# Kernel optimization log

Measured on AMD Instinct MI355X. Metric: run time of the kernel, lower is better.

## Reference

```python
import math
import jax, jax.numpy as jnp
import numpy as np

N_QUBITS = 16
BATCH = 128
N_STATE = 2 ** N_QUBITS


def cnot_ring(n_qubits):
    """Permutation equivalent to a CNOT ring (faithful copy of the torch repo's numpy code)."""
    n2 = np.array([0, 2, 3, 1])
    if n_qubits == 2:
        return n2
    evens = np.zeros(2 ** (n_qubits - 1))
    answer = n2[::2]
    for i in range(1, n_qubits - 1):
        evens[:2 ** i] = answer
        a, b = np.array_split(answer, 2)
        evens[2 ** i:2 ** i + 2 ** (i - 1)] = a + 3 * 2 ** i
        evens[2 ** i + 2 ** (i - 1):2 ** (i + 1)] = b + 2 ** i
        answer = evens[:2 ** (i + 1)]
    a, b = np.split(evens.copy() + 2 ** (n_qubits - 2), 2)
    a = np.mod(a, 2 ** (n_qubits - 1))
    b, c = np.split(b, 2)
    b = b - 2 ** (n_qubits - 1)
    odds = np.concatenate((a, b, c), axis=0)[::-1]
    output = np.zeros(2 ** n_qubits)
    output[::2] = evens
    output[1::2] = odds
    return output.astype(int)


def binary_mask(n_qubits):
    """[n, 2**n] matrix; row i is bit (n-1-i from LSB) of the column index,
    matching torch binary_matrix (dim 0 of the [2]*n tensor is the MSB)."""
    idx = jnp.arange(2 ** n_qubits, dtype=jnp.int32)
    shifts = (n_qubits - 1 - jnp.arange(n_qubits, dtype=jnp.int32))
    return ((idx[None, :] >> shifts[:, None]) & 1).astype(jnp.float32)


def wht(x):
    """Walsh-Hadamard transform over the last dim of [B, N] complex state (had_big butterfly)."""
    B, N = x.shape
    n = int(math.log2(N))
    for i in range(n):
        x = x.reshape(B, 2 ** i, 2, N >> (i + 1))
        a, b = x[:, :, 0, :], x[:, :, 1, :]
        x = jnp.stack([a + b, a - b], axis=2)
    return x.reshape(B, N) * jnp.asarray(2.0 ** (-n / 2), dtype=x.dtype)


def setup_inputs() -> dict:
    key = jax.random.key(0)
    k1, k2, k3 = jax.random.split(key, 3)
    state_re = jax.random.normal(k1, (BATCH, N_STATE), dtype=jnp.float32)
    state_im = jax.random.normal(k2, (BATCH, N_STATE), dtype=jnp.float32)
    thetas = jax.random.normal(k3, (BATCH, N_QUBITS), dtype=jnp.float32)
    cnot_p = jnp.asarray(cnot_ring(N_QUBITS), dtype=jnp.int32)
    return {"state_re": state_re, "state_im": state_im, "thetas": thetas, "cnot_p": cnot_p}


def reference(state_re, state_im, thetas, cnot_p):
    # set_state('random'): l2-normalize complex state per batch row
    norm = jnp.sqrt(jnp.sum(state_re * state_re + state_im * state_im, axis=-1, keepdims=True))
    state = (state_re + 1j * state_im) / norm  # complex64 [B, N]
    # hadamard layer (had_big WHT butterfly)
    state = wht(state)
    # RZ layer: thetas @ binary mask -> phase eigenvalues exp(-i*theta/2)
    ang = thetas @ binary_mask(N_QUBITS)  # [B, N]
    state = state * jnp.exp(-0.5j * ang)
    # CNOT ring: gather permutation over the state axis
    state = state[:, cnot_p]
    # second hadamard layer
    state = wht(state)
    # measure(): probabilities |psi|^2
    return jnp.abs(state) ** 2
```

## Files before the change

kernel.cpp:

```cpp
#include <hip/hip_runtime.h>
#include <hip/hip_fp16.h>

#define NB 128
#define NS 65536

typedef float v2f __attribute__((ext_vector_type(2)));

__device__ __forceinline__ v2f pk_fma(v2f a, v2f b, v2f c) {
  v2f d;
  asm("v_pk_fma_f32 %0, %1, %2, %3" : "=v"(d) : "v"(a), "v"(b), "v"(c));
  return d;
}
__device__ __forceinline__ v2f pk_add(v2f a, v2f b) {
  v2f d;
  asm("v_pk_add_f32 %0, %1, %2" : "=v"(d) : "v"(a), "v"(b));
  return d;
}
__device__ __forceinline__ v2f pk_mul(v2f a, v2f b) {
  v2f d;
  asm("v_pk_mul_f32 %0, %1, %2" : "=v"(d) : "v"(a), "v"(b));
  return d;
}

template <int CTRL>
__device__ __forceinline__ float dppmov(float x) {
  return __int_as_float(__builtin_amdgcn_update_dpp(
      0, __float_as_int(x), CTRL, 0xF, 0xF, false));
}
__device__ __forceinline__ float xor4mov(float x) {
  int t = __builtin_amdgcn_update_dpp(0, __float_as_int(x), 0x104, 0xF, 0x5, false);
  t = __builtin_amdgcn_update_dpp(t, __float_as_int(x), 0x114, 0xF, 0xA, false);
  return __int_as_float(t);
}

__device__ __forceinline__ void wht256p(v2f (&p)[4], int lane) {
  const v2f M1 = {-1.f, -1.f};
  {
    v2f t;
    t = p[0]; p[0] = pk_add(t, p[1]); p[1] = pk_fma(M1, p[1], t);
    t = p[2]; p[2] = pk_add(t, p[3]); p[3] = pk_fma(M1, p[3], t);
    t = p[0]; p[0] = pk_add(t, p[2]); p[2] = pk_fma(M1, p[2], t);
    t = p[1]; p[1] = pk_add(t, p[3]); p[3] = pk_fma(M1, p[3], t);
  }
  const float s1f  = (lane & 1)  ? -1.f : 1.f;
  const float s2f  = (lane & 2)  ? -1.f : 1.f;
  const float s4f  = (lane & 4)  ? -1.f : 1.f;
  const float s8f  = (lane & 8)  ? -1.f : 1.f;
  const float s16f = (lane & 16) ? -1.f : 1.f;
  const float s32f = (lane & 32) ? -1.f : 1.f;
  const v2f s1 = {s1f, s1f}, s2 = {s2f, s2f}, s4 = {s4f, s4f};
  const v2f s8 = {s8f, s8f}, s16 = {s16f, s16f}, s32 = {s32f, s32f};
#pragma unroll
  for (int q = 0; q < 4; ++q) {
    v2f m = {dppmov<0xB1>(p[q].x), dppmov<0xB1>(p[q].y)};
    p[q] = pk_fma(s1, p[q], m);
  }
#pragma unroll
  for (int q = 0; q < 4; ++q) {
    v2f m = {dppmov<0x4E>(p[q].x), dppmov<0x4E>(p[q].y)};
    p[q] = pk_fma(s2, p[q], m);
  }
#pragma unroll
  for (int q = 0; q < 4; ++q) {
    v2f m = {xor4mov(p[q].x), xor4mov(p[q].y)};
    p[q] = pk_fma(s4, p[q], m);
  }
#pragma unroll
  for (int q = 0; q < 4; ++q) {
    v2f m = {dppmov<0x128>(p[q].x), dppmov<0x128>(p[q].y)};
    p[q] = pk_fma(s8, p[q], m);
  }
#pragma unroll
  for (int q = 0; q < 4; ++q) {
    auto rre = __builtin_amdgcn_permlane16_swap(__float_as_uint(p[q].x),
                                                __float_as_uint(p[q].x), false, false);
    auto rim = __builtin_amdgcn_permlane16_swap(__float_as_uint(p[q].y),
                                                __float_as_uint(p[q].y), false, false);
    v2f lo = {__uint_as_float(rre[0]), __uint_as_float(rim[0])};
    v2f hi = {__uint_as_float(rre[1]), __uint_as_float(rim[1])};
    p[q] = pk_fma(s16, hi, lo);
  }
#pragma unroll
  for (int q = 0; q < 4; ++q) {
    auto rre = __builtin_amdgcn_permlane32_swap(__float_as_uint(p[q].x),
                                                __float_as_uint(p[q].x), false, false);
    auto rim = __builtin_amdgcn_permlane32_swap(__float_as_uint(p[q].y),
                                                __float_as_uint(p[q].y), false, false);
    v2f lo = {__uint_as_float(rre[0]), __uint_as_float(rim[0])};
    v2f hi = {__uint_as_float(rre[1]), __uint_as_float(rim[1])};
    p[q] = pk_fma(s32, hi, lo);
  }
}

__global__ __launch_bounds__(1024, 8) void k1_ahi(const float* __restrict__ sre,
                                                  const float* __restrict__ sim,
                                                  const float* __restrict__ thetas,
                                                  __half* __restrict__ T,
                                                  float* __restrict__ partial) {
  __shared__ float sr[32][260];
  __shared__ float si[32][260];
  __shared__ float2 phh4[64];
  __shared__ float2 phHQ[4];
  __shared__ float red[16];
  const int bid = blockIdx.x;
  const int b = bid >> 3, tile = bid & 7;
  const int lo0 = tile * 32;
  const int tid = threadIdx.x, lane = tid & 63, w = tid >> 6;
  if (tid < 64) {
    const float* tb = thetas + b * 16;
    float a = 0.f;
#pragma unroll
    for (int i = 0; i < 6; ++i)
      if ((tid >> (5 - i)) & 1) a += tb[i];
    phh4[tid] = make_float2(cosf(0.5f * a), -sinf(0.5f * a));
    if (tid < 4) {
      float aq = 0.f;
      if (tid & 1) aq += tb[7];
      if (tid & 2) aq += tb[6];
      phHQ[tid] = make_float2(cosf(0.5f * aq), -sinf(0.5f * aq));
    }
  }
  const float* pre = sre + ((size_t)b << 16);
  const float* pim = sim + ((size_t)b << 16);
  const int c = tid & 7, jr = tid >> 3;
  const int j0 = jr, j1 = jr + 128;
  const float4 vr0 = *reinterpret_cast<const float4*>(pre + j0 * 256 + lo0 + c * 4);
  const float4 vi0 = *reinterpret_cast<const float4*>(pim + j0 * 256 + lo0 + c * 4);
  const float4 vr1 = *reinterpret_cast<const float4*>(pre + j1 * 256 + lo0 + c * 4);
  const float4 vi1 = *reinterpret_cast<const float4*>(pim + j1 * 256 + lo0 + c * 4);
  float acc = vr0.x*vr0.x + vr0.y*vr0.y + vr0.z*vr0.z + vr0.w*vr0.w
            + vi0.x*vi0.x + vi0.y*vi0.y + vi0.z*vi0.z + vi0.w*vi0.w
            + vr1.x*vr1.x + vr1.y*vr1.y + vr1.z*vr1.z + vr1.w*vr1.w
            + vi1.x*vi1.x + vi1.y*vi1.y + vi1.z*vi1.z + vi1.w*vi1.w;
  {
    const int fs = ((c >> 1) & 3) << 2;
    const int j0s = j0 ^ fs, j1s = j1 ^ fs;
    sr[c*4+0][j0s] = vr0.x; sr[c*4+1][j0s] = vr0.y; sr[c*4+2][j0s] = vr0.z; sr[c*4+3][j0s] = vr0.w;
    si[c*4+0][j0s] = vi0.x; si[c*4+1][j0s] = vi0.y; si[c*4+2][j0s] = vi0.z; si[c*4+3][j0s] = vi0.w;
    sr[c*4+0][j1s] = vr1.x; sr[c*4+1][j1s] = vr1.y; sr[c*4+2][j1s] = vr1.z; sr[c*4+3][j1s] = vr1.w;
    si[c*4+0][j1s] = vi1.x; si[c*4+1][j1s] = vi1.y; si[c*4+2][j1s] = vi1.z; si[c*4+3][j1s] = vi1.w;
  }
#pragma unroll
  for (int m2 = 32; m2 >= 1; m2 >>= 1) acc += __shfl_xor(acc, m2, 64);
  if (lane == 0) red[w] = acc;
  __syncthreads();
  if (tid == 0) {
    float sm = 0.f;
#pragma unroll
    for (int k = 0; k < 16; ++k) sm += red[k];
    partial[bid] = sm;
  }
  const float2 p4 = phh4[lane];
  float prq[4], piq[4];
#pragma unroll
  for (int q = 0; q < 4; ++q) {
    const float2 pq = phHQ[q];
    prq[q] = p4.x * pq.x - p4.y * pq.y;
    piq[q] = p4.x * pq.y + p4.y * pq.x;
  }
#pragma unroll
  for (int r = 0; r < 2; ++r) {
    const int ll = w * 2 + r;
    const int blk = lane ^ ((ll >> 3) & 3);
    const float4 a4 = *reinterpret_cast<const float4*>(&sr[ll][blk * 4]);
    const float4 b4 = *reinterpret_cast<const float4*>(&si[ll][blk * 4]);
    v2f p[4] = {{a4.x, b4.x}, {a4.y, b4.y}, {a4.z, b4.z}, {a4.w, b4.w}};
    wht256p(p, lane);
#pragma unroll
    for (int q = 0; q < 4; ++q) {
      const float ur = p[q].x, ui = p[q].y;
      const v2f tt = pk_mul(p[q], (v2f){prq[q], prq[q]});
      p[q].x = fmaf(-piq[q], ui, tt.x);
      p[q].y = fmaf(piq[q], ur, tt.y);
    }
    wht256p(p, lane);
    *reinterpret_cast<float4*>(&sr[ll][blk * 4]) =
        make_float4(p[0].x, p[1].x, p[2].x, p[3].x);
    *reinterpret_cast<float4*>(&si[ll][blk * 4]) =
        make_float4(p[0].y, p[1].y, p[2].y, p[3].y);
  }
  __syncthreads();
  __half* Tb = T + ((size_t)b << 17);
  const int m = tid >> 2, sub = tid & 3;
  const int ms = m ^ (sub << 2);
  unsigned int o8[8];
#pragma unroll
  for (int t = 0; t < 8; ++t) {
    const int ll = 8 * sub + t;
    const __half2 h = __floats2half2_rn(sr[ll][ms], si[ll][ms]);
    o8[t] = *reinterpret_cast<const unsigned int*>(&h);
  }
  __half* dst = Tb + ((size_t)m << 9) + (size_t)(lo0 + 8 * sub) * 2;
  *reinterpret_cast<uint4*>(dst) = make_uint4(o8[0], o8[1], o8[2], o8[3]);
  *reinterpret_cast<uint4*>(dst + 8) = make_uint4(o8[4], o8[5], o8[6], o8[7]);
}

__global__ __launch_bounds__(256, 8) void k2_alo_scatter(const __half* __restrict__ T,
                                                         const float* __restrict__ thetas,
                                                         const int* __restrict__ cnot,
                                                         const float* __restrict__ partial,
                                                         float* __restrict__ outp) {
  __shared__ float2 phl4[64];
  __shared__ float2 phLQ[4];
  __shared__ int sloL[64];
  __shared__ int tj[16];
  __shared__ int srow16[16];
  __shared__ float th[16];
  __shared__ float shinv;
  const int bid = blockIdx.x;
  const int x = bid & 7, s2i = bid >> 3;
  const int b = x * 16 + (s2i >> 4), tile = s2i & 15;
  const int tid = threadIdx.x, lane = tid & 63, w = tid >> 6;
  if (tid < 16) {
    th[tid] = thetas[b * 16 + tid];
    int v = 0;
#pragma unroll
    for (int i = 0; i < 16; ++i) v |= ((cnot[1 << i] >> tid) & 1) << i;
    tj[tid] = v;
  }
  if (tid == 0) {
    float sum = 0.f;
#pragma unroll
    for (int k = 0; k < 8; ++k) sum += partial[b * 8 + k];
    shinv = 1.0f / (sum * 4294967296.0f);
  }
  __syncthreads();
  if (tid < 64) {
    float a = 0.f;
#pragma unroll
    for (int i = 0; i < 6; ++i)
      if ((tid >> (5 - i)) & 1) a += th[8 + i];
    phl4[tid] = make_float2(cosf(0.5f * a), -sinf(0.5f * a));
    int v = 0;
#pragma unroll
    for (int bb = 0; bb < 6; ++bb)
      if ((tid >> bb) & 1) v ^= tj[2 + bb];
    sloL[tid] = v;
    if (tid < 4) {
      float aq = 0.f;
      if (tid & 1) aq += th[15];
      if (tid & 2) aq += th[14];
      phLQ[tid] = make_float2(cosf(0.5f * aq), -sinf(0.5f * aq));
    }
  }
  if (tid < 16) {
    const int mh = tile * 16 + tid;
    int v = 0;
#pragma unroll
    for (int bb = 0; bb < 8; ++bb)
      if ((mh >> bb) & 1) v ^= tj[8 + bb];
    srow16[tid] = v;
  }
  __syncthreads();
  const __half* Tb = T + ((size_t)b << 17);
  float* ob = outp + ((size_t)b << 16);
  const float iv = shinv;
  const float2 p4 = phl4[lane];
  const int sL = sloL[lane];
  const int sq1 = tj[0], sq2 = tj[1], sq3 = tj[0] ^ tj[1];
  float prq[4], piq[4];
#pragma unroll
  for (int q = 0; q < 4; ++q) {
    const float2 pq = phLQ[q];
    prq[q] = p4.x * pq.x - p4.y * pq.y;
    piq[q] = p4.x * pq.y + p4.y * pq.x;
  }
#pragma unroll
  for (int r = 0; r < 4; ++r) {
    const int rl = w * 4 + r;
    const int mh = tile * 16 + rl;
    const uint4 hv = *reinterpret_cast<const uint4*>(Tb + ((size_t)mh << 9) + lane * 8);
    const float2 f0 = __half22float2(*reinterpret_cast<const __half2*>(&hv.x));
    const float2 f1 = __half22float2(*reinterpret_cast<const __half2*>(&hv.y));
    const float2 f2 = __half22float2(*reinterpret_cast<const __half2*>(&hv.z));
    const float2 f3 = __half22float2(*reinterpret_cast<const __half2*>(&hv.w));
    v2f p[4] = {{f0.x, f0.y}, {f1.x, f1.y}, {f2.x, f2.y}, {f3.x, f3.y}};
    wht256p(p, lane);
#pragma unroll
    for (int q = 0; q < 4; ++q) {
      const float ur = p[q].x, ui = p[q].y;
      const v2f tt = pk_mul(p[q], (v2f){prq[q], prq[q]});
      p[q].x = fmaf(-piq[q], ui, tt.x);
      p[q].y = fmaf(piq[q], ur, tt.y);
    }
    wht256p(p, lane);
    const int base = srow16[rl] ^ sL;
    const v2f m0 = pk_mul(p[0], p[0]);
    const v2f m1 = pk_mul(p[1], p[1]);
    const v2f m2 = pk_mul(p[2], p[2]);
    const v2f m3 = pk_mul(p[3], p[3]);
    ob[base]       = (m0.x + m0.y) * iv;
    ob[base ^ sq1] = (m1.x + m1.y) * iv;
    ob[base ^ sq2] = (m2.x + m2.y) * iv;
    ob[base ^ sq3] = (m3.x + m3.y) * iv;
  }
}

extern "C" void kernel_launch(void* const* d_in, const int* in_sizes, int n_in,
                              void* d_out, int out_size, void* d_ws, size_t ws_size,
                              hipStream_t stream) {
  const float* sre = (const float*)d_in[0];
  const float* sim = (const float*)d_in[1];
  const float* thetas = (const float*)d_in[2];
  const int* cnot = (const int*)d_in[3];
  float* outp = (float*)d_out;
  char* w = (char*)d_ws;
  const size_t HPLANE = (size_t)NB * NS * 2 * sizeof(__half);
  if (ws_size < HPLANE + 8192) return;
  __half* T = (__half*)(w);
  float* partial = (float*)(w + HPLANE);

  hipLaunchKernelGGL(k1_ahi, dim3(1024), dim3(1024), 0, stream, sre, sim, thetas, T, partial);
  hipLaunchKernelGGL(k2_alo_scatter, dim3(2048), dim3(256), 0, stream, T, thetas, cnot, partial, outp);
}
```

Measured before the change: 59.82 us.

## Pack k1 shared staging to half2 and halve k1 block size

The first kernel now stages its 32x256 tile in shared memory as packed half2 (re,im) words in a single padded array, replacing the two fp32 arrays. This halves LDS footprint and traffic. It also moves to 512-thread blocks where each thread loads four rows and processes four WHT rows, and uses packed FMA for the norm accumulation. The cost is that values are rounded to fp16 before the first WHT and phase instead of after, which adds precision loss to that stage. The XOR swizzle is dropped in favour of plain padding, which may change bank-conflict behaviour.

```diff
diff --git a/kernel.cpp b/kernel.cpp
--- a/kernel.cpp
+++ b/kernel.cpp
@@ -3,6 +3,7 @@
 
 #define NB 128
 #define NS 65536
+#define LP 260
 
 typedef float v2f __attribute__((ext_vector_type(2)));
 
@@ -92,16 +93,24 @@
   }
 }
 
-__global__ __launch_bounds__(1024, 8) void k1_ahi(const float* __restrict__ sre,
-                                                  const float* __restrict__ sim,
-                                                  const float* __restrict__ thetas,
-                                                  __half* __restrict__ T,
-                                                  float* __restrict__ partial) {
-  __shared__ float sr[32][260];
-  __shared__ float si[32][260];
+__device__ __forceinline__ unsigned int pack2(float re, float im) {
+  const __half2 h = __floats2half2_rn(re, im);
+  return *reinterpret_cast<const unsigned int*>(&h);
+}
+__device__ __forceinline__ v2f unpack2(unsigned int u) {
+  const float2 f = __half22float2(*reinterpret_cast<const __half2*>(&u));
+  return (v2f){f.x, f.y};
+}
+
+__global__ __launch_bounds__(512, 8) void k1_ahi(const float* __restrict__ sre,
+                                                 const float* __restrict__ sim,
+                                                 const float* __restrict__ thetas,
+                                                 __half* __restrict__ T,
+                                                 float* __restrict__ partial) {
+  __shared__ unsigned int sh[32 * LP];
   __shared__ float2 phh4[64];
   __shared__ float2 phHQ[4];
-  __shared__ float red[16];
+  __shared__ float red[8];
   const int bid = blockIdx.x;
   const int b = bid >> 3, tile = bid & 7;
   const int lo0 = tile * 32;
@@ -123,23 +132,27 @@
   const float* pre = sre + ((size_t)b << 16);
   const float* pim = sim + ((size_t)b << 16);
   const int c = tid & 7, jr = tid >> 3;
-  const int j0 = jr, j1 = jr + 128;
-  const float4 vr0 = *reinterpret_cast<const float4*>(pre + j0 * 256 + lo0 + c * 4);
-  const float4 vi0 = *reinterpret_cast<const float4*>(pim + j0 * 256 + lo0 + c * 4);
-  const float4 vr1 = *reinterpret_cast<const float4*>(pre + j1 * 256 + lo0 + c * 4);
-  const float4 vi1 = *reinterpret_cast<const float4*>(pim + j1 * 256 + lo0 + c * 4);
-  float acc = vr0.x*vr0.x + vr0.y*vr0.y + vr0.z*vr0.z + vr0.w*vr0.w
-            + vi0.x*vi0.x + vi0.y*vi0.y + vi0.z*vi0.z + vi0.w*vi0.w
-            + vr1.x*vr1.x + vr1.y*vr1.y + vr1.z*vr1.z + vr1.w*vr1.w
-            + vi1.x*vi1.x + vi1.y*vi1.y + vi1.z*vi1.z + vi1.w*vi1.w;
-  {
-    const int fs = ((c >> 1) & 3) << 2;
-    const int j0s = j0 ^ fs, j1s = j1 ^ fs;
-    sr[c*4+0][j0s] = vr0.x; sr[c*4+1][j0s] = vr0.y; sr[c*4+2][j0s] = vr0.z; sr[c*4+3][j0s] = vr0.w;
-    si[c*4+0][j0s] = vi0.x; si[c*4+1][j0s] = vi0.y; si[c*4+2][j0s] = vi0.z; si[c*4+3][j0s] = vi0.w;
-    sr[c*4+0][j1s] = vr1.x; sr[c*4+1][j1s] = vr1.y; sr[c*4+2][j1s] = vr1.z; sr[c*4+3][j1s] = vr1.w;
-    si[c*4+0][j1s] = vi1.x; si[c*4+1][j1s] = vi1.y; si[c*4+2][j1s] = vi1.z; si[c*4+3][j1s] = vi1.w;
-  }
+  float4 vr[4], vi[4];
+#pragma unroll
+  for (int it = 0; it < 4; ++it) {
+    const int j = jr + it * 64;
+    vr[it] = *reinterpret_cast<const float4*>(pre + j * 256 + lo0 + c * 4);
+    vi[it] = *reinterpret_cast<const float4*>(pim + j * 256 + lo0 + c * 4);
+  }
+  v2f acc2 = {0.f, 0.f};
+#pragma unroll
+  for (int it = 0; it < 4; ++it) {
+    v2f u0 = {vr[it].x, vi[it].x}, u1 = {vr[it].y, vi[it].y};
+    v2f u2 = {vr[it].z, vi[it].z}, u3 = {vr[it].w, vi[it].w};
+    acc2 = pk_fma(u0, u0, acc2); acc2 = pk_fma(u1, u1, acc2);
+    acc2 = pk_fma(u2, u2, acc2); acc2 = pk_fma(u3, u3, acc2);
+    const int j = jr + it * 64;
+    sh[(c * 4 + 0) * LP + j] = pack2(vr[it].x, vi[it].x);
+    sh[(c * 4 + 1) * LP + j] = pack2(vr[it].y, vi[it].y);
+    sh[(c * 4 + 2) * LP + j] = pack2(vr[it].z, vi[it].z);
+    sh[(c * 4 + 3) * LP + j] = pack2(vr[it].w, vi[it].w);
+  }
+  float acc = acc2.x + acc2.y;
 #pragma unroll
   for (int m2 = 32; m2 >= 1; m2 >>= 1) acc += __shfl_xor(acc, m2, 64);
   if (lane == 0) red[w] = acc;
@@ -147,7 +160,7 @@
   if (tid == 0) {
     float sm = 0.f;
 #pragma unroll
-    for (int k = 0; k < 16; ++k) sm += red[k];
+    for (int k = 0; k < 8; ++k) sm += red[k];
     partial[bid] = sm;
   }
   const float2 p4 = phh4[lane];
@@ -159,12 +172,10 @@
     piq[q] = p4.x * pq.y + p4.y * pq.x;
   }
 #pragma unroll
-  for (int r = 0; r < 2; ++r) {
-    const int ll = w * 2 + r;
-    const int blk = lane ^ ((ll >> 3) & 3);
-    const float4 a4 = *reinterpret_cast<const float4*>(&sr[ll][blk * 4]);
-    const float4 b4 = *reinterpret_cast<const float4*>(&si[ll][blk * 4]);
-    v2f p[4] = {{a4.x, b4.x}, {a4.y, b4.y}, {a4.z, b4.z}, {a4.w, b4.w}};
+  for (int r = 0; r < 4; ++r) {
+    const int row = w * 4 + r;
+    uint4 hv = *reinterpret_cast<const uint4*>(&sh[row * LP + lane * 4]);
+    v2f p[4] = {unpack2(hv.x), unpack2(hv.y), unpack2(hv.z), unpack2(hv.w)};
     wht256p(p, lane);
 #pragma unroll
     for (int q = 0; q < 4; ++q) {
@@ -174,25 +185,21 @@
       p[q].y = fmaf(piq[q], ur, tt.y);
     }
     wht256p(p, lane);
-    *reinterpret_cast<float4*>(&sr[ll][blk * 4]) =
-        make_float4(p[0].x, p[1].x, p[2].x, p[3].x);
-    *reinterpret_cast<float4*>(&si[ll][blk * 4]) =
-        make_float4(p[0].y, p[1].y, p[2].y, p[3].y);
+    hv.x = pack2(p[0].x, p[0].y); hv.y = pack2(p[1].x, p[1].y);
+    hv.z = pack2(p[2].x, p[2].y); hv.w = pack2(p[3].x, p[3].y);
+    *reinterpret_cast<uint4*>(&sh[row * LP + lane * 4]) = hv;
   }
   __syncthreads();
   __half* Tb = T + ((size_t)b << 17);
-  const int m = tid >> 2, sub = tid & 3;
-  const int ms = m ^ (sub << 2);
-  unsigned int o8[8];
-#pragma unroll
-  for (int t = 0; t < 8; ++t) {
-    const int ll = 8 * sub + t;
-    const __half2 h = __floats2half2_rn(sr[ll][ms], si[ll][ms]);
-    o8[t] = *reinterpret_cast<const unsigned int*>(&h);
-  }
-  __half* dst = Tb + ((size_t)m << 9) + (size_t)(lo0 + 8 * sub) * 2;
-  *reinterpret_cast<uint4*>(dst) = make_uint4(o8[0], o8[1], o8[2], o8[3]);
-  *reinterpret_cast<uint4*>(dst + 8) = make_uint4(o8[4], o8[5], o8[6], o8[7]);
+  const int m = tid >> 1, h = tid & 1;
+  unsigned int o[16];
+#pragma unroll
+  for (int t = 0; t < 16; ++t) o[t] = sh[(16 * h + t) * LP + m];
+  __half* dst = Tb + ((size_t)m << 9) + (size_t)(lo0 + 16 * h) * 2;
+  *reinterpret_cast<uint4*>(dst)      = make_uint4(o[0], o[1], o[2], o[3]);
+  *reinterpret_cast<uint4*>(dst + 8)  = make_uint4(o[4], o[5], o[6], o[7]);
+  *reinterpret_cast<uint4*>(dst + 16) = make_uint4(o[8], o[9], o[10], o[11]);
+  *reinterpret_cast<uint4*>(dst + 24) = make_uint4(o[12], o[13], o[14], o[15]);
 }
 
 __global__ __launch_bounds__(256, 8) void k2_alo_scatter(const __half* __restrict__ T,
@@ -270,11 +277,7 @@
     const int rl = w * 4 + r;
     const int mh = tile * 16 + rl;
     const uint4 hv = *reinterpret_cast<const uint4*>(Tb + ((size_t)mh << 9) + lane * 8);
-    const float2 f0 = __half22float2(*reinterpret_cast<const __half2*>(&hv.x));
-    const float2 f1 = __half22float2(*reinterpret_cast<const __half2*>(&hv.y));
-    const float2 f2 = __half22float2(*reinterpret_cast<const __half2*>(&hv.z));
-    const float2 f3 = __half22float2(*reinterpret_cast<const __half2*>(&hv.w));
-    v2f p[4] = {{f0.x, f0.y}, {f1.x, f1.y}, {f2.x, f2.y}, {f3.x, f3.y}};
+    v2f p[4] = {unpack2(hv.x), unpack2(hv.y), unpack2(hv.z), unpack2(hv.w)};
     wht256p(p, lane);
 #pragma unroll
     for (int q = 0; q < 4; ++q) {
@@ -310,6 +313,6 @@
   __half* T = (__half*)(w);
   float* partial = (float*)(w + HPLANE);
 
-  hipLaunchKernelGGL(k1_ahi, dim3(1024), dim3(1024), 0, stream, sre, sim, thetas, T, partial);
+  hipLaunchKernelGGL(k1_ahi, dim3(1024), dim3(512), 0, stream, sre, sim, thetas, T, partial);
   hipLaunchKernelGGL(k2_alo_scatter, dim3(2048), dim3(256), 0, stream, T, thetas, cnot, partial, outp);
 }
```

Result: slower. 61.56 us (+2.9%).
